# Performance work log

Hardware: AMD Instinct MI355X
Metric: run time of the kernel (lower is better)

The kernel has to match this reference:

```python
import jax, jax.numpy as jnp
import numpy as np

EPS = 1e-5

def _layernorm(x, g, b):
    m = jnp.mean(x, axis=-1, keepdims=True)
    v = jnp.var(x, axis=-1, keepdims=True)
    return (x - m) * jax.lax.rsqrt(v + EPS) * g + b

def setup_inputs() -> dict:
    key = jax.random.key(0)
    ks = jax.random.split(key, 8)
    B, N, D, H = 4, 2048, 1024, 16
    F = 2 * D
    s = 0.02
    return {
        "x": jax.random.normal(ks[0], (B, N, D), jnp.float32),
        "mask": jnp.zeros((B, N, N), jnp.float32),
        "Wq": jax.random.normal(ks[1], (D, D), jnp.float32) * s,
        "Wk": jax.random.normal(ks[2], (D, D), jnp.float32) * s,
        "Wv": jax.random.normal(ks[3], (D, D), jnp.float32) * s,
        "Wc": jax.random.normal(ks[4], (D, D), jnp.float32) * s,
        "bc": jnp.zeros((D,), jnp.float32),
        "W1": jax.random.normal(ks[5], (D, F), jnp.float32) * s,
        "b1": jnp.zeros((F,), jnp.float32),
        "W2": jax.random.normal(ks[6], (F, D), jnp.float32) * s,
        "b2": jnp.zeros((D,), jnp.float32),
        "g1": jnp.ones((D,), jnp.float32),
        "be1": jnp.zeros((D,), jnp.float32),
        "g2": jnp.ones((D,), jnp.float32),
        "be2": jnp.zeros((D,), jnp.float32),
    }

def reference(x, mask, Wq, Wk, Wv, Wc, bc, W1, b1, W2, b2, g1, be1, g2, be2):
    B, N, D = x.shape
    H = 16
    Dh = D // H
    scale = 1.0 / np.sqrt(Dh).astype(np.float32)
    # projections -> [B, H, N, Dh]
    def heads(t):
        return t.reshape(B, N, H, Dh).transpose(0, 2, 1, 3)
    q = heads(x @ Wq)
    k = heads(x @ Wk)
    v = heads(x @ Wv)
    score = jnp.einsum('bhnd,bhmd->bhnm', q, k) * scale + mask[:, None, :, :]
    attn = jnp.einsum('bhnm,bhmd->bhnd', jax.nn.softmax(score, axis=-1), v)
    attn = attn.transpose(0, 2, 1, 3).reshape(B, N, D)
    x = x + attn @ Wc + bc
    x = _layernorm(x, g1, be1)
    x = x + jnp.maximum(x @ W1 + b1, 0.0) @ W2 + b2
    x = _layernorm(x, g2, be2)
    return x
```

## Files before the change

kernel.cpp:

```cpp
#include <hip/hip_runtime.h>
#include <hip/hip_bf16.h>


#define DEV __device__ __forceinline__

using s16x8  = __attribute__((ext_vector_type(8))) short;
using f32x4  = __attribute__((ext_vector_type(4))) float;

DEV unsigned short f2bf(float f) {
  unsigned u = __float_as_uint(f);
  u += 0x7fffu + ((u >> 16) & 1u);
  return (unsigned short)(u >> 16);
}
DEV unsigned cvt_pk_bf16(float lo, float hi) {
  unsigned r;
  asm("v_cvt_pk_bf16_f32 %0, %1, %2" : "=v"(r) : "v"(lo), "v"(hi));
  return r;
}
DEV float bf2f(unsigned short b) { return __uint_as_float((unsigned)b << 16); }

typedef __attribute__((address_space(3))) unsigned lds_u32_t;
typedef const __attribute__((address_space(1))) unsigned glb_u32_t;

DEV void gld_lds16(const void* g, void* l) {
  __builtin_amdgcn_global_load_lds((glb_u32_t*)g, (lds_u32_t*)l, 16, 0, 0);
}

template<int RELU, int VOUT, int SPLITK>
__global__ __launch_bounds__(512, 2)
void gemm8p(const unsigned short* __restrict__ A, const unsigned short* __restrict__ Bt,
            unsigned short* __restrict__ Cb, const float* __restrict__ bias,
            unsigned short* __restrict__ vtout, int M, int N, int K)
{
  __shared__ unsigned short Sh[2][2][256 * 64];
  const int tid = threadIdx.x;
  const int w = tid >> 6, lane = tid & 63;
  const int g = lane >> 4, q = lane & 15;
  const int wr = w >> 2, wc = w & 3;

  const int nwg  = gridDim.x * gridDim.y;
  const int flat = blockIdx.y * gridDim.x + blockIdx.x;
  const int rm   = (flat & 7) * (nwg >> 3) + (flat >> 3);
  int m0, n0, kz = 0;
  if (SPLITK) {
    kz = rm >> 7;
    const int sp = rm & 127;
    m0 = (sp >> 2) * 256; n0 = (sp & 3) * 256;
  } else {
    m0 = (rm / gridDim.x) * 256; n0 = (rm % gridDim.x) * 256;
  }

  f32x4 acc[8][4] = {};

  const int srow = w * 8 + (lane >> 3);
  const int scol = ((lane & 7) ^ (lane >> 3)) * 8;
  const unsigned short* Ag = A  + (size_t)(m0 + srow) * K + scol + (SPLITK ? kz * (K >> 1) : 0);
  const unsigned short* Bg = Bt + (size_t)(n0 + srow) * K + scol + (SPLITK ? kz * (K >> 1) : 0);

  auto STG = [&](const unsigned short* Gb, int buf, int ab, int half, int kt) {
    const unsigned short* gs = Gb + (size_t)(half * 128) * K + kt * 64;
    unsigned short* ls = &Sh[buf][ab][(half * 128 + w * 8) * 64];
    gld_lds16(gs, ls);
    gld_lds16(gs + (size_t)64 * K, ls + 64 * 64);
  };
  auto LDA = [&](int buf, int mq, s16x8 af[4][2]) {
#pragma unroll
    for (int mm = 0; mm < 4; ++mm) {
      const unsigned short* rp = &Sh[buf][0][(wr * 128 + mq * 64 + mm * 16 + q) * 64];
#pragma unroll
      for (int kk = 0; kk < 2; ++kk)
        af[mm][kk] = *(const s16x8*)(rp + (((kk * 4 + g) ^ (q & 7)) * 8));
    }
  };
  auto LDB = [&](int buf, int nq, s16x8 bf[2][2]) {
#pragma unroll
    for (int nn = 0; nn < 2; ++nn) {
      const unsigned short* rp = &Sh[buf][1][(wc * 64 + nq * 32 + nn * 16 + q) * 64];
#pragma unroll
      for (int kk = 0; kk < 2; ++kk)
        bf[nn][kk] = *(const s16x8*)(rp + (((kk * 4 + g) ^ (q & 7)) * 8));
    }
  };
  auto MQ = [&](int mq, int nq, const s16x8 af[4][2], const s16x8 bf[2][2]) {
    __builtin_amdgcn_s_setprio(1);
#pragma unroll
    for (int kk = 0; kk < 2; ++kk)
#pragma unroll
      for (int mm = 0; mm < 4; ++mm)
#pragma unroll
        for (int nn = 0; nn < 2; ++nn)
          acc[mq * 4 + mm][nq * 2 + nn] = __builtin_amdgcn_mfma_f32_16x16x32_bf16(
              af[mm][kk], bf[nn][kk], acc[mq * 4 + mm][nq * 2 + nn], 0, 0, 0);
    __builtin_amdgcn_s_setprio(0);
  };
  auto BAR = [&]() { __builtin_amdgcn_sched_barrier(0); __builtin_amdgcn_s_barrier(); };

  STG(Ag, 0, 0, 0, 0); STG(Ag, 0, 0, 1, 0);
  STG(Bg, 0, 1, 0, 0); STG(Bg, 0, 1, 1, 0);

  const int NKT = SPLITK ? (K >> 7) : (K >> 6);
  s16x8 af[4][2], bf0[2][2], bf1[2][2];
#pragma unroll 1
  for (int kt = 0; kt < NKT; ++kt) {
    const int b = kt & 1, sb = b ^ 1, kn = kt + 1;
    const bool stg = (kn < NKT);
    if (stg) { STG(Ag, sb, 0, 0, kn); asm volatile("s_waitcnt vmcnt(2)" ::: "memory"); }
    else     {                        asm volatile("s_waitcnt vmcnt(0)" ::: "memory"); }
    BAR();
    LDA(b, 0, af); LDB(b, 0, bf0);
    MQ(0, 0, af, bf0);
    BAR();
    if (stg) STG(Ag, sb, 0, 1, kn);
    LDB(b, 1, bf1);
    MQ(0, 1, af, bf1);
    BAR();
    if (stg) STG(Bg, sb, 1, 0, kn);
    LDA(b, 1, af);
    MQ(1, 0, af, bf0);
    BAR();
    if (stg) STG(Bg, sb, 1, 1, kn);
    MQ(1, 1, af, bf1);
    BAR();
  }

#pragma unroll
  for (int n = 0; n < 4; ++n) {
    const int col = n0 + wc * 64 + n * 16 + q;
    if (SPLITK) {
      unsigned short* Cp = Cb + (size_t)kz * M * N;
#pragma unroll
      for (int m = 0; m < 8; ++m) {
        const int row0 = m0 + wr * 128 + m * 16 + g * 4;
#pragma unroll
        for (int r = 0; r < 4; ++r)
          Cp[(size_t)(row0 + r) * N + col] = f2bf(acc[m][n][r]);
      }
    } else if (VOUT && col >= 2048) {
      const int cv = col - 2048;
#pragma unroll
      for (int m = 0; m < 8; ++m) {
        const int row0 = m0 + wr * 128 + m * 16 + g * 4;
        const int bb = row0 >> 11;
        ushort4 pk;
        pk.x = f2bf(acc[m][n][0]); pk.y = f2bf(acc[m][n][1]);
        pk.z = f2bf(acc[m][n][2]); pk.w = f2bf(acc[m][n][3]);
        *(ushort4*)(vtout + ((size_t)bb * 1024 + cv) * 2048 + (row0 & 2047)) = pk;
      }
    } else {
      const float scl = (VOUT && col < 1024) ? 0.18033688011112042f : 1.0f;
      const float bv = bias ? bias[col] : 0.0f;
#pragma unroll
      for (int m = 0; m < 8; ++m) {
        const int row0 = m0 + wr * 128 + m * 16 + g * 4;
#pragma unroll
        for (int r = 0; r < 4; ++r) {
          float v = acc[m][n][r] * scl + bv;
          if (RELU) v = fmaxf(v, 0.0f);
          Cb[(size_t)(row0 + r) * N + col] = f2bf(v);
        }
      }
    }
  }
}

template<int RELU, int RESID, int OUTF>
__global__ __launch_bounds__(256)
void gemm_bt(const unsigned short* __restrict__ A, const unsigned short* __restrict__ Bt,
             unsigned short* __restrict__ Cb, float* __restrict__ Cf,
             const float* __restrict__ bias, const float* __restrict__ resid,
             const unsigned short* __restrict__ residb,
             int M, int N, int K)
{
  __shared__ unsigned short As[2][4096];
  __shared__ unsigned short Bs[2][4096];
  const int tid  = threadIdx.x;
  const int wave = tid >> 6, lane = tid & 63;
  const int g = lane >> 4, q = lane & 15;

  const int nwg  = gridDim.x * gridDim.y;
  const int flat = blockIdx.y * gridDim.x + blockIdx.x;
  const int rm   = (nwg & 7) ? flat : ((flat & 7) * (nwg >> 3) + (flat >> 3));
  const int m0 = (rm / gridDim.x) * 128, n0 = (rm % gridDim.x) * 128;
  const int wr = wave >> 1, wc = wave & 1;

  f32x4 acc[4][4] = {};

  const int i0 = wave * 512 + lane * 8;
  const int i1 = 2048 + i0;

  auto STAGE = [&](int buf, int kt) {
    gld_lds16(A  + (size_t)(m0 + (i0 >> 5)) * K + kt + (i0 & 31), As[buf] + wave * 512);
    gld_lds16(Bt + (size_t)(n0 + (i0 >> 5)) * K + kt + (i0 & 31), Bs[buf] + wave * 512);
    gld_lds16(A  + (size_t)(m0 + (i1 >> 5)) * K + kt + (i1 & 31), As[buf] + 2048 + wave * 512);
    gld_lds16(Bt + (size_t)(n0 + (i1 >> 5)) * K + kt + (i1 & 31), Bs[buf] + 2048 + wave * 512);
  };

  STAGE(0, 0);
  __syncthreads();
  int cur = 0;
#pragma unroll 1
  for (int kt = 0; kt < K; kt += 32) {
    if (kt + 32 < K) STAGE(cur ^ 1, kt + 32);
    s16x8 a[4], b[4];
#pragma unroll
    for (int m = 0; m < 4; ++m)
      a[m] = *(const s16x8*)(As[cur] + (wr * 64 + m * 16 + q) * 32 + g * 8);
#pragma unroll
    for (int n = 0; n < 4; ++n)
      b[n] = *(const s16x8*)(Bs[cur] + (wc * 64 + n * 16 + q) * 32 + g * 8);
    __builtin_amdgcn_s_setprio(1);
#pragma unroll
    for (int m = 0; m < 4; ++m)
#pragma unroll
      for (int n = 0; n < 4; ++n)
        acc[m][n] = __builtin_amdgcn_mfma_f32_16x16x32_bf16(a[m], b[n], acc[m][n], 0, 0, 0);
    __builtin_amdgcn_s_setprio(0);
    __syncthreads();
    cur ^= 1;
  }

#pragma unroll
  for (int n = 0; n < 4; ++n) {
    const int col = n0 + wc * 64 + n * 16 + q;
    const float bv = bias ? bias[col] : 0.0f;
#pragma unroll
    for (int m = 0; m < 4; ++m) {
      const int row0 = m0 + wr * 64 + m * 16 + g * 4;
#pragma unroll
      for (int r = 0; r < 4; ++r) {
        float v = acc[m][n][r] + bv;
        if (RELU) v = fmaxf(v, 0.0f);
        if (RESID == 2) v += bf2f(residb[(size_t)(row0 + r) * N + col]);
        if (OUTF) Cf[(size_t)(row0 + r) * N + col] = v;
        else      Cb[(size_t)(row0 + r) * N + col] = f2bf(v);
      }
    }
  }
}

__global__ __launch_bounds__(256, 4)
void attn_kernel(const unsigned short* __restrict__ qkv,
                 const unsigned short* __restrict__ vt,
                 const float* __restrict__ mask,
                 unsigned short* __restrict__ outb)
{
  __shared__ unsigned short Ks[2][4096];
  __shared__ unsigned short Vs[2][4096];
  const int tid = threadIdx.x, wave = tid >> 6, lane = tid & 63;
  const int g = lane >> 4, q = lane & 15;

  const int flat = blockIdx.y * 32 + blockIdx.x;
  const int rm   = (flat & 7) * 256 + (flat >> 3);
  const int h  = rm & 15;
  const int qt = (rm >> 4) & 31;
  const int b  = rm >> 9;
  const int qrow = qt * 64 + wave * 16;
  const size_t tok0 = (size_t)b * 2048;

  const unsigned short* Qp = qkv + (tok0 + qrow + q) * 3072 + h * 64;
  const s16x8 bq0 = *(const s16x8*)(Qp + g * 8);
  const s16x8 bq1 = *(const s16x8*)(Qp + 32 + g * 8);
  const float* Mp = mask + ((size_t)b * 2048 + qrow + q) * 2048 + g * 4;

  const int lr = lane >> 3;
  const int sc = (lane & 7) ^ lr;
  const unsigned short* Kg = qkv + tok0 * 3072 + 1024 + h * 64
                           + (size_t)(wave * 16 + lr) * 3072 + sc * 8;
  const unsigned short* Vg = vt + (((size_t)b * 16 + h) * 64 + wave * 16 + lr) * 2048 + sc * 8;
  unsigned short* KsW = Ks[0] + wave * 1024;
  unsigned short* VsW = Vs[0] + wave * 1024;

  s16x8 ones;
#pragma unroll
  for (int j = 0; j < 8; ++j) ones[j] = (short)0x3F80;

  f32x4 ot[4] = {};
  f32x4 sacc = {};
  f32x4 mk0[4], mk1[4];
  const float L2E = 1.4426950408889634f;

  gld_lds16(Kg,            KsW);
  gld_lds16(Kg + 8 * 3072, KsW + 512);
  gld_lds16(Vg,            VsW);
  gld_lds16(Vg + 8 * 2048, VsW + 512);
#pragma unroll
  for (int m2 = 0; m2 < 4; ++m2) {
    const f32x4 r = *(const f32x4*)(Mp + m2 * 16);
#pragma unroll
    for (int i = 0; i < 4; ++i) mk0[m2][i] = fmaf(r[i], L2E, -8.0f);
  }
  __syncthreads();

#define ATTN_TILE(BUF, MKC, MKN, STG)                                          \
  {                                                                            \
    f32x4 mu[4];                                                               \
    if (STG) {                                                                 \
      Kg += 64 * 3072; Vg += 64; Mp += 64;                                     \
      gld_lds16(Kg,            KsW + (BUF ^ 1) * 4096);                        \
      gld_lds16(Kg + 8 * 3072, KsW + (BUF ^ 1) * 4096 + 512);                  \
      gld_lds16(Vg,            VsW + (BUF ^ 1) * 4096);                        \
      gld_lds16(Vg + 8 * 2048, VsW + (BUF ^ 1) * 4096 + 512);                  \
      mu[0] = *(const f32x4*)(Mp);      mu[1] = *(const f32x4*)(Mp + 16);      \
      mu[2] = *(const f32x4*)(Mp + 32); mu[3] = *(const f32x4*)(Mp + 48);      \
    }                                                                          \
    __builtin_amdgcn_s_setprio(1);                                             \
    _Pragma("unroll")                                                          \
    for (int m2 = 0; m2 < 4; ++m2) {                                           \
      const unsigned short* kp = Ks[BUF] + (m2 * 16 + q) * 64;                 \
      const s16x8 ak0 = *(const s16x8*)(kp + ((g       ^ (q & 7)) * 8));       \
      const s16x8 ak1 = *(const s16x8*)(kp + (((g + 4) ^ (q & 7)) * 8));       \
      MKC[m2] = __builtin_amdgcn_mfma_f32_16x16x32_bf16(ak0, bq0, MKC[m2], 0, 0, 0); \
      MKC[m2] = __builtin_amdgcn_mfma_f32_16x16x32_bf16(ak1, bq1, MKC[m2], 0, 0, 0); \
    }                                                                          \
    __builtin_amdgcn_s_setprio(0);                                             \
    uint2 pkk[4];                                                              \
    _Pragma("unroll")                                                          \
    for (int m2 = 0; m2 < 4; ++m2) {                                           \
      MKC[m2][0] = exp2f(MKC[m2][0]); MKC[m2][1] = exp2f(MKC[m2][1]);          \
      MKC[m2][2] = exp2f(MKC[m2][2]); MKC[m2][3] = exp2f(MKC[m2][3]);          \
      pkk[m2].x = cvt_pk_bf16(MKC[m2][0], MKC[m2][1]);                         \
      pkk[m2].y = cvt_pk_bf16(MKC[m2][2], MKC[m2][3]);                         \
    }                                                                          \
    __builtin_amdgcn_sched_barrier(0);                                         \
    __builtin_amdgcn_s_barrier();           \
    char* Pw = (char*)(&Ks[BUF][0]) + wave * 2048;                             \
    _Pragma("unroll")                                                          \
    for (int m2 = 0; m2 < 4; ++m2) {                                           \
      const int bir  = m2 * 32 + g * 8;                                        \
      const int addr = q * 128 + (((bir >> 4) ^ (q & 7)) << 4) + (bir & 15);   \
      *(uint2*)(Pw + addr) = pkk[m2];                                          \
    }                                                                          \
    __builtin_amdgcn_s_setprio(1);                                             \
    _Pragma("unroll")                                                          \
    for (int kb = 0; kb < 2; ++kb) {                                           \
      const int blk = (kb * 4 + g) ^ (q & 7);                                  \
      const s16x8 pb = *(const s16x8*)(Pw + q * 128 + blk * 16);               \
      sacc = __builtin_amdgcn_mfma_f32_16x16x32_bf16(ones, pb, sacc, 0, 0, 0); \
      _Pragma("unroll")                                                        \
      for (int mm = 0; mm < 4; ++mm) {                                         \
        const s16x8 av = *(const s16x8*)(Vs[BUF] + (mm * 16 + q) * 64 + blk * 8); \
        ot[mm] = __builtin_amdgcn_mfma_f32_16x16x32_bf16(av, pb, ot[mm], 0, 0, 0); \
      }                                                                        \
    }                                                                          \
    __builtin_amdgcn_s_setprio(0);                                             \
    if (STG) {                                                                 \
      _Pragma("unroll")                                                        \
      for (int m2 = 0; m2 < 4; ++m2) {                                         \
        MKN[m2][0] = fmaf(mu[m2][0], L2E, -8.0f);                              \
        MKN[m2][1] = fmaf(mu[m2][1], L2E, -8.0f);                              \
        MKN[m2][2] = fmaf(mu[m2][2], L2E, -8.0f);                              \
        MKN[m2][3] = fmaf(mu[m2][3], L2E, -8.0f);                              \
      }                                                                        \
    }                                                                          \
    __syncthreads();                                                           \
  }

#pragma unroll 1
  for (int tt = 0; tt < 16; ++tt) {
    ATTN_TILE(0, mk0, mk1, true);
    ATTN_TILE(1, mk1, mk0, (tt < 15));
  }
#undef ATTN_TILE

  char* Pw0 = (char*)(&Ks[0][0]) + wave * 2048;
  const float inv = 1.0f / sacc[0];
#pragma unroll
  for (int mm = 0; mm < 4; ++mm) {
    const int bir  = mm * 32 + g * 8;
    const int addr = q * 128 + (((bir >> 4) ^ (q & 7)) << 4) + (bir & 15);
    uint2 pk;
    pk.x = cvt_pk_bf16(ot[mm][0] * inv, ot[mm][1] * inv);
    pk.y = cvt_pk_bf16(ot[mm][2] * inv, ot[mm][3] * inv);
    *(uint2*)(Pw0 + addr) = pk;
  }
#pragma unroll
  for (int p = 0; p < 2; ++p) {
    const int c  = p * 64 + lane;
    const int qq = c >> 3, cc = c & 7;
    const int blk = cc ^ (qq & 7);
    const s16x8 vv = *(const s16x8*)(Pw0 + qq * 128 + blk * 16);
    *(s16x8*)(outb + (tok0 + qrow + qq) * 1024 + h * 64 + cc * 8) = vv;
  }
}

template<int MODE>
__global__ __launch_bounds__(256)
void ln_kernel(const unsigned short* __restrict__ inb,
               const unsigned short* __restrict__ p0, const unsigned short* __restrict__ p1,
               const float* __restrict__ bias, const unsigned short* __restrict__ residb,
               float* __restrict__ outf, unsigned short* __restrict__ outb,
               const float* __restrict__ gam, const float* __restrict__ bet)
{
  __shared__ float red[8];
  const int row = blockIdx.x, tid = threadIdx.x;
  const size_t base = (size_t)row * 1024 + tid * 4;
  f32x4 v;
  if (MODE == 0) {
    const uint2 u = *(const uint2*)(inb + base);
    v[0] = __uint_as_float(u.x << 16); v[1] = __uint_as_float(u.x & 0xffff0000u);
    v[2] = __uint_as_float(u.y << 16); v[3] = __uint_as_float(u.y & 0xffff0000u);
  } else {
    const uint2 a = *(const uint2*)(p0 + base);
    const uint2 c = *(const uint2*)(p1 + base);
    const f32x4 bs = *(const f32x4*)(bias + tid * 4);
    const uint2 u = *(const uint2*)(residb + base);
    v[0] = __uint_as_float(a.x << 16)         + __uint_as_float(c.x << 16)
         + bs[0] + __uint_as_float(u.x << 16);
    v[1] = __uint_as_float(a.x & 0xffff0000u) + __uint_as_float(c.x & 0xffff0000u)
         + bs[1] + __uint_as_float(u.x & 0xffff0000u);
    v[2] = __uint_as_float(a.y << 16)         + __uint_as_float(c.y << 16)
         + bs[2] + __uint_as_float(u.y << 16);
    v[3] = __uint_as_float(a.y & 0xffff0000u) + __uint_as_float(c.y & 0xffff0000u)
         + bs[3] + __uint_as_float(u.y & 0xffff0000u);
  }
  float s  = v[0] + v[1] + v[2] + v[3];
  float ss = v[0]*v[0] + v[1]*v[1] + v[2]*v[2] + v[3]*v[3];
#pragma unroll
  for (int o = 1; o < 64; o <<= 1) { s += __shfl_xor(s, o); ss += __shfl_xor(ss, o); }
  if ((tid & 63) == 0) { red[tid >> 6] = s; red[4 + (tid >> 6)] = ss; }
  __syncthreads();
  s  = red[0] + red[1] + red[2] + red[3];
  ss = red[4] + red[5] + red[6] + red[7];
  const float mean = s * (1.0f / 1024.0f);
  const float var  = ss * (1.0f / 1024.0f) - mean * mean;
  const float rstd = rsqrtf(var + 1e-5f);
  const f32x4 gm = *(const f32x4*)(gam + tid * 4);
  const f32x4 bt = *(const f32x4*)(bet + tid * 4);
  f32x4 o;
#pragma unroll
  for (int j = 0; j < 4; ++j) o[j] = (v[j] - mean) * rstd * gm[j] + bt[j];
  if (outf) *(f32x4*)(outf + base) = o;
  if (outb) {
    uint2 pk; pk.x = cvt_pk_bf16(o[0], o[1]); pk.y = cvt_pk_bf16(o[2], o[3]);
    *(uint2*)(outb + base) = pk;
  }
}

__global__ __launch_bounds__(256)
void prep_kernel(const float* __restrict__ x, unsigned short* __restrict__ xb,
                 const float* __restrict__ Wq, const float* __restrict__ Wk,
                 const float* __restrict__ Wv, const float* __restrict__ Wc,
                 const float* __restrict__ W1, const float* __restrict__ W2,
                 unsigned short* __restrict__ wqkvt, unsigned short* __restrict__ wct,
                 unsigned short* __restrict__ w1t, unsigned short* __restrict__ w2t)
{
  const int bid = blockIdx.x;
  if (bid < 8192) {
    const size_t i = ((size_t)bid * 256 + threadIdx.x) * 4;
    const f32x4 v = *(const f32x4*)(x + i);
    uint2 pk; pk.x = cvt_pk_bf16(v[0], v[1]); pk.y = cvt_pk_bf16(v[2], v[3]);
    *(uint2*)(xb + i) = pk;
    return;
  }
  __shared__ float t[32][33];
  const int t2 = bid - 8192;
  const float* in; unsigned short* out; int R, C, bx, by;
  if (t2 < 4096) {
    const int widx = t2 >> 10, sub = t2 & 1023;
    in  = (widx == 0) ? Wq : (widx == 1) ? Wk : (widx == 2) ? Wv : Wc;
    out = (widx < 3) ? (wqkvt + (size_t)widx * 1024 * 1024) : wct;
    R = 1024; C = 1024; bx = sub & 31; by = sub >> 5;
  } else if (t2 < 6144) {
    const int sub = t2 - 4096;
    in = W1; out = w1t; R = 1024; C = 2048; bx = sub & 63; by = sub >> 6;
  } else {
    const int sub = t2 - 6144;
    in = W2; out = w2t; R = 2048; C = 1024; bx = sub & 31; by = sub >> 5;
  }
  const int tx = threadIdx.x & 31, ty = threadIdx.x >> 5;
  const int c0 = bx * 32, r0 = by * 32;
#pragma unroll
  for (int k = 0; k < 4; ++k)
    t[ty + k * 8][tx] = in[(size_t)(r0 + ty + k * 8) * C + c0 + tx];
  __syncthreads();
#pragma unroll
  for (int k = 0; k < 4; ++k)
    out[(size_t)(c0 + ty + k * 8) * R + r0 + tx] = f2bf(t[tx][ty + k * 8]);
}

extern "C" void kernel_launch(void* const* d_in, const int* in_sizes, int n_in,
                              void* d_out, int out_size, void* d_ws, size_t ws_size,
                              hipStream_t stream)
{
  (void)in_sizes; (void)n_in; (void)out_size; (void)ws_size;
  const float* x   = (const float*)d_in[0];
  const float* msk = (const float*)d_in[1];
  const float* Wq  = (const float*)d_in[2];
  const float* Wk  = (const float*)d_in[3];
  const float* Wv  = (const float*)d_in[4];
  const float* Wc  = (const float*)d_in[5];
  const float* bc  = (const float*)d_in[6];
  const float* W1  = (const float*)d_in[7];
  const float* b1  = (const float*)d_in[8];
  const float* W2  = (const float*)d_in[9];
  const float* b2  = (const float*)d_in[10];
  const float* g1  = (const float*)d_in[11];
  const float* be1 = (const float*)d_in[12];
  const float* g2  = (const float*)d_in[13];
  const float* be2 = (const float*)d_in[14];
  float* out = (float*)d_out;
  char* ws = (char*)d_ws;
  const size_t MB = 1u << 20;
  unsigned short* xb    = (unsigned short*)(ws + 0 * MB);
  unsigned short* wqkvt = (unsigned short*)(ws + 16 * MB);
  unsigned short* wct   = (unsigned short*)(ws + 22 * MB);
  unsigned short* w1t   = (unsigned short*)(ws + 24 * MB);
  unsigned short* w2t   = (unsigned short*)(ws + 28 * MB);
  unsigned short* qkv   = (unsigned short*)(ws + 32 * MB);
  unsigned short* vt    = (unsigned short*)(ws + 80 * MB);
  unsigned short* attnb = (unsigned short*)(ws + 96 * MB);
  unsigned short* y1b   = (unsigned short*)(ws + 112 * MB);
  unsigned short* h1b   = (unsigned short*)(ws + 128 * MB);
  unsigned short* midb  = (unsigned short*)(ws + 32 * MB);
  unsigned short* pffb  = (unsigned short*)(ws + 64 * MB);

  prep_kernel<<<16384, 256, 0, stream>>>(x, xb, Wq, Wk, Wv, Wc, W1, W2,
                                         wqkvt, wct, w1t, w2t);
  gemm8p<0, 1, 0><<<dim3(12, 32), 512, 0, stream>>>(xb, wqkvt, qkv, nullptr, vt,
                                                    8192, 3072, 1024);
  attn_kernel<<<dim3(32, 64), 256, 0, stream>>>(qkv, vt, msk, attnb);
  gemm_bt<0, 2, 0><<<dim3(8, 64), 256, 0, stream>>>(attnb, wct, y1b, nullptr,
                                                    bc, nullptr, xb, 8192, 1024, 1024);
  ln_kernel<0><<<8192, 256, 0, stream>>>(y1b, nullptr, nullptr, nullptr, nullptr,
                                         nullptr, h1b, g1, be1);
  gemm8p<1, 0, 0><<<dim3(8, 32), 512, 0, stream>>>(h1b, w1t, midb, b1, nullptr,
                                                   8192, 2048, 1024);
  gemm8p<0, 0, 1><<<dim3(8, 32), 512, 0, stream>>>(midb, w2t, pffb, nullptr, nullptr,
                                                   8192, 1024, 2048);
  ln_kernel<1><<<8192, 256, 0, stream>>>(nullptr, pffb, pffb + (size_t)8192 * 1024,
                                         b2, h1b, out, nullptr, g2, be2);
}
```

Measured before the change: 397.7 us.

## Widen attention tiles to 8 waves and route out-projection through split-K gemm8p

The attention kernel now uses 512-thread blocks covering 128 query rows. Each wave loads half as much K/V per tile, and each wave gets its own LDS scratch for P, which removes the extra barrier that came from reusing the K buffer. The output projection drops the 128x128 gemm_bt kernel and uses the gemm8p split-K path, writing two partial bf16 halves. A single unified ln_kernel then sums the halves with bias and residual before the layernorm. LDS use per block grows, and the split-K path costs extra write and read traffic for the partials.

```diff
diff --git a/kernel.cpp b/kernel.cpp
--- a/kernel.cpp
+++ b/kernel.cpp
@@ -163,82 +163,7 @@
   }
 }
 
-template<int RELU, int RESID, int OUTF>
-__global__ __launch_bounds__(256)
-void gemm_bt(const unsigned short* __restrict__ A, const unsigned short* __restrict__ Bt,
-             unsigned short* __restrict__ Cb, float* __restrict__ Cf,
-             const float* __restrict__ bias, const float* __restrict__ resid,
-             const unsigned short* __restrict__ residb,
-             int M, int N, int K)
-{
-  __shared__ unsigned short As[2][4096];
-  __shared__ unsigned short Bs[2][4096];
-  const int tid  = threadIdx.x;
-  const int wave = tid >> 6, lane = tid & 63;
-  const int g = lane >> 4, q = lane & 15;
-
-  const int nwg  = gridDim.x * gridDim.y;
-  const int flat = blockIdx.y * gridDim.x + blockIdx.x;
-  const int rm   = (nwg & 7) ? flat : ((flat & 7) * (nwg >> 3) + (flat >> 3));
-  const int m0 = (rm / gridDim.x) * 128, n0 = (rm % gridDim.x) * 128;
-  const int wr = wave >> 1, wc = wave & 1;
-
-  f32x4 acc[4][4] = {};
-
-  const int i0 = wave * 512 + lane * 8;
-  const int i1 = 2048 + i0;
-
-  auto STAGE = [&](int buf, int kt) {
-    gld_lds16(A  + (size_t)(m0 + (i0 >> 5)) * K + kt + (i0 & 31), As[buf] + wave * 512);
-    gld_lds16(Bt + (size_t)(n0 + (i0 >> 5)) * K + kt + (i0 & 31), Bs[buf] + wave * 512);
-    gld_lds16(A  + (size_t)(m0 + (i1 >> 5)) * K + kt + (i1 & 31), As[buf] + 2048 + wave * 512);
-    gld_lds16(Bt + (size_t)(n0 + (i1 >> 5)) * K + kt + (i1 & 31), Bs[buf] + 2048 + wave * 512);
-  };
-
-  STAGE(0, 0);
-  __syncthreads();
-  int cur = 0;
-#pragma unroll 1
-  for (int kt = 0; kt < K; kt += 32) {
-    if (kt + 32 < K) STAGE(cur ^ 1, kt + 32);
-    s16x8 a[4], b[4];
-#pragma unroll
-    for (int m = 0; m < 4; ++m)
-      a[m] = *(const s16x8*)(As[cur] + (wr * 64 + m * 16 + q) * 32 + g * 8);
-#pragma unroll
-    for (int n = 0; n < 4; ++n)
-      b[n] = *(const s16x8*)(Bs[cur] + (wc * 64 + n * 16 + q) * 32 + g * 8);
-    __builtin_amdgcn_s_setprio(1);
-#pragma unroll
-    for (int m = 0; m < 4; ++m)
-#pragma unroll
-      for (int n = 0; n < 4; ++n)
-        acc[m][n] = __builtin_amdgcn_mfma_f32_16x16x32_bf16(a[m], b[n], acc[m][n], 0, 0, 0);
-    __builtin_amdgcn_s_setprio(0);
-    __syncthreads();
-    cur ^= 1;
-  }
-
-#pragma unroll
-  for (int n = 0; n < 4; ++n) {
-    const int col = n0 + wc * 64 + n * 16 + q;
-    const float bv = bias ? bias[col] : 0.0f;
-#pragma unroll
-    for (int m = 0; m < 4; ++m) {
-      const int row0 = m0 + wr * 64 + m * 16 + g * 4;
-#pragma unroll
-      for (int r = 0; r < 4; ++r) {
-        float v = acc[m][n][r] + bv;
-        if (RELU) v = fmaxf(v, 0.0f);
-        if (RESID == 2) v += bf2f(residb[(size_t)(row0 + r) * N + col]);
-        if (OUTF) Cf[(size_t)(row0 + r) * N + col] = v;
-        else      Cb[(size_t)(row0 + r) * N + col] = f2bf(v);
-      }
-    }
-  }
-}
-
-__global__ __launch_bounds__(256, 4)
+__global__ __launch_bounds__(512, 6)
 void attn_kernel(const unsigned short* __restrict__ qkv,
                  const unsigned short* __restrict__ vt,
                  const float* __restrict__ mask,
@@ -246,15 +171,16 @@
 {
   __shared__ unsigned short Ks[2][4096];
   __shared__ unsigned short Vs[2][4096];
+  __shared__ unsigned short Pl[8][1024];
   const int tid = threadIdx.x, wave = tid >> 6, lane = tid & 63;
   const int g = lane >> 4, q = lane & 15;
 
-  const int flat = blockIdx.y * 32 + blockIdx.x;
-  const int rm   = (flat & 7) * 256 + (flat >> 3);
+  const int flat = blockIdx.y * 16 + blockIdx.x;
+  const int rm   = (flat & 7) * 128 + (flat >> 3);
   const int h  = rm & 15;
-  const int qt = (rm >> 4) & 31;
-  const int b  = rm >> 9;
-  const int qrow = qt * 64 + wave * 16;
+  const int qt = (rm >> 4) & 15;
+  const int b  = rm >> 8;
+  const int qrow = qt * 128 + wave * 16;
   const size_t tok0 = (size_t)b * 2048;
 
   const unsigned short* Qp = qkv + (tok0 + qrow + q) * 3072 + h * 64;
@@ -265,10 +191,10 @@
   const int lr = lane >> 3;
   const int sc = (lane & 7) ^ lr;
   const unsigned short* Kg = qkv + tok0 * 3072 + 1024 + h * 64
-                           + (size_t)(wave * 16 + lr) * 3072 + sc * 8;
-  const unsigned short* Vg = vt + (((size_t)b * 16 + h) * 64 + wave * 16 + lr) * 2048 + sc * 8;
-  unsigned short* KsW = Ks[0] + wave * 1024;
-  unsigned short* VsW = Vs[0] + wave * 1024;
+                           + (size_t)(wave * 8 + lr) * 3072 + sc * 8;
+  const unsigned short* Vg = vt + (((size_t)b * 16 + h) * 64 + wave * 8 + lr) * 2048 + sc * 8;
+  unsigned short* KsW = Ks[0] + wave * 512;
+  unsigned short* VsW = Vs[0] + wave * 512;
 
   s16x8 ones;
 #pragma unroll
@@ -277,12 +203,11 @@
   f32x4 ot[4] = {};
   f32x4 sacc = {};
   f32x4 mk0[4], mk1[4];
+  char* Pw = (char*)&Pl[wave][0];
   const float L2E = 1.4426950408889634f;
 
-  gld_lds16(Kg,            KsW);
-  gld_lds16(Kg + 8 * 3072, KsW + 512);
-  gld_lds16(Vg,            VsW);
-  gld_lds16(Vg + 8 * 2048, VsW + 512);
+  gld_lds16(Kg, KsW);
+  gld_lds16(Vg, VsW);
 #pragma unroll
   for (int m2 = 0; m2 < 4; ++m2) {
     const f32x4 r = *(const f32x4*)(Mp + m2 * 16);
@@ -296,10 +221,8 @@
     f32x4 mu[4];                                                               \
     if (STG) {                                                                 \
       Kg += 64 * 3072; Vg += 64; Mp += 64;                                     \
-      gld_lds16(Kg,            KsW + (BUF ^ 1) * 4096);                        \
-      gld_lds16(Kg + 8 * 3072, KsW + (BUF ^ 1) * 4096 + 512);                  \
-      gld_lds16(Vg,            VsW + (BUF ^ 1) * 4096);                        \
-      gld_lds16(Vg + 8 * 2048, VsW + (BUF ^ 1) * 4096 + 512);                  \
+      gld_lds16(Kg, KsW + (BUF ^ 1) * 4096);                                   \
+      gld_lds16(Vg, VsW + (BUF ^ 1) * 4096);                                   \
       mu[0] = *(const f32x4*)(Mp);      mu[1] = *(const f32x4*)(Mp + 16);      \
       mu[2] = *(const f32x4*)(Mp + 32); mu[3] = *(const f32x4*)(Mp + 48);      \
     }                                                                          \
@@ -313,22 +236,16 @@
       MKC[m2] = __builtin_amdgcn_mfma_f32_16x16x32_bf16(ak1, bq1, MKC[m2], 0, 0, 0); \
     }                                                                          \
     __builtin_amdgcn_s_setprio(0);                                             \
-    uint2 pkk[4];                                                              \
     _Pragma("unroll")                                                          \
     for (int m2 = 0; m2 < 4; ++m2) {                                           \
       MKC[m2][0] = exp2f(MKC[m2][0]); MKC[m2][1] = exp2f(MKC[m2][1]);          \
       MKC[m2][2] = exp2f(MKC[m2][2]); MKC[m2][3] = exp2f(MKC[m2][3]);          \
-      pkk[m2].x = cvt_pk_bf16(MKC[m2][0], MKC[m2][1]);                         \
-      pkk[m2].y = cvt_pk_bf16(MKC[m2][2], MKC[m2][3]);                         \
-    }                                                                          \
-    __builtin_amdgcn_sched_barrier(0);                                         \
-    __builtin_amdgcn_s_barrier();           \
-    char* Pw = (char*)(&Ks[BUF][0]) + wave * 2048;                             \
-    _Pragma("unroll")                                                          \
-    for (int m2 = 0; m2 < 4; ++m2) {                                           \
       const int bir  = m2 * 32 + g * 8;                                        \
       const int addr = q * 128 + (((bir >> 4) ^ (q & 7)) << 4) + (bir & 15);   \
-      *(uint2*)(Pw + addr) = pkk[m2];                                          \
+      uint2 pk;                                                                \
+      pk.x = cvt_pk_bf16(MKC[m2][0], MKC[m2][1]);                              \
+      pk.y = cvt_pk_bf16(MKC[m2][2], MKC[m2][3]);                              \
+      *(uint2*)(Pw + addr) = pk;                        \
     }                                                                          \
     __builtin_amdgcn_s_setprio(1);                                             \
     _Pragma("unroll")                                                          \
@@ -352,7 +269,7 @@
         MKN[m2][3] = fmaf(mu[m2][3], L2E, -8.0f);                              \
       }                                                                        \
     }                                                                          \
-    __syncthreads();                                                           \
+    __syncthreads();                            \
   }
 
 #pragma unroll 1
@@ -362,7 +279,6 @@
   }
 #undef ATTN_TILE
 
-  char* Pw0 = (char*)(&Ks[0][0]) + wave * 2048;
   const float inv = 1.0f / sacc[0];
 #pragma unroll
   for (int mm = 0; mm < 4; ++mm) {
@@ -371,22 +287,20 @@
     uint2 pk;
     pk.x = cvt_pk_bf16(ot[mm][0] * inv, ot[mm][1] * inv);
     pk.y = cvt_pk_bf16(ot[mm][2] * inv, ot[mm][3] * inv);
-    *(uint2*)(Pw0 + addr) = pk;
+    *(uint2*)(Pw + addr) = pk;
   }
 #pragma unroll
   for (int p = 0; p < 2; ++p) {
     const int c  = p * 64 + lane;
     const int qq = c >> 3, cc = c & 7;
     const int blk = cc ^ (qq & 7);
-    const s16x8 vv = *(const s16x8*)(Pw0 + qq * 128 + blk * 16);
+    const s16x8 vv = *(const s16x8*)(Pw + qq * 128 + blk * 16);
     *(s16x8*)(outb + (tok0 + qrow + qq) * 1024 + h * 64 + cc * 8) = vv;
   }
 }
 
-template<int MODE>
 __global__ __launch_bounds__(256)
-void ln_kernel(const unsigned short* __restrict__ inb,
-               const unsigned short* __restrict__ p0, const unsigned short* __restrict__ p1,
+void ln_kernel(const unsigned short* __restrict__ p0, const unsigned short* __restrict__ p1,
                const float* __restrict__ bias, const unsigned short* __restrict__ residb,
                float* __restrict__ outf, unsigned short* __restrict__ outb,
                const float* __restrict__ gam, const float* __restrict__ bet)
@@ -394,25 +308,19 @@
   __shared__ float red[8];
   const int row = blockIdx.x, tid = threadIdx.x;
   const size_t base = (size_t)row * 1024 + tid * 4;
+  const uint2 a = *(const uint2*)(p0 + base);
+  const uint2 c = *(const uint2*)(p1 + base);
+  const f32x4 bs = *(const f32x4*)(bias + tid * 4);
+  const uint2 u = *(const uint2*)(residb + base);
   f32x4 v;
-  if (MODE == 0) {
-    const uint2 u = *(const uint2*)(inb + base);
-    v[0] = __uint_as_float(u.x << 16); v[1] = __uint_as_float(u.x & 0xffff0000u);
-    v[2] = __uint_as_float(u.y << 16); v[3] = __uint_as_float(u.y & 0xffff0000u);
-  } else {
-    const uint2 a = *(const uint2*)(p0 + base);
-    const uint2 c = *(const uint2*)(p1 + base);
-    const f32x4 bs = *(const f32x4*)(bias + tid * 4);
-    const uint2 u = *(const uint2*)(residb + base);
-    v[0] = __uint_as_float(a.x << 16)         + __uint_as_float(c.x << 16)
-         + bs[0] + __uint_as_float(u.x << 16);
-    v[1] = __uint_as_float(a.x & 0xffff0000u) + __uint_as_float(c.x & 0xffff0000u)
-         + bs[1] + __uint_as_float(u.x & 0xffff0000u);
-    v[2] = __uint_as_float(a.y << 16)         + __uint_as_float(c.y << 16)
-         + bs[2] + __uint_as_float(u.y << 16);
-    v[3] = __uint_as_float(a.y & 0xffff0000u) + __uint_as_float(c.y & 0xffff0000u)
-         + bs[3] + __uint_as_float(u.y & 0xffff0000u);
-  }
+  v[0] = __uint_as_float(a.x << 16)         + __uint_as_float(c.x << 16)
+       + bs[0] + __uint_as_float(u.x << 16);
+  v[1] = __uint_as_float(a.x & 0xffff0000u) + __uint_as_float(c.x & 0xffff0000u)
+       + bs[1] + __uint_as_float(u.x & 0xffff0000u);
+  v[2] = __uint_as_float(a.y << 16)         + __uint_as_float(c.y << 16)
+       + bs[2] + __uint_as_float(u.y << 16);
+  v[3] = __uint_as_float(a.y & 0xffff0000u) + __uint_as_float(c.y & 0xffff0000u)
+       + bs[3] + __uint_as_float(u.y & 0xffff0000u);
   float s  = v[0] + v[1] + v[2] + v[3];
   float ss = v[0]*v[0] + v[1]*v[1] + v[2]*v[2] + v[3]*v[3];
 #pragma unroll
@@ -509,8 +417,8 @@
   unsigned short* qkv   = (unsigned short*)(ws + 32 * MB);
   unsigned short* vt    = (unsigned short*)(ws + 80 * MB);
   unsigned short* attnb = (unsigned short*)(ws + 96 * MB);
-  unsigned short* y1b   = (unsigned short*)(ws + 112 * MB);
   unsigned short* h1b   = (unsigned short*)(ws + 128 * MB);
+  unsigned short* prb   = (unsigned short*)(ws + 32 * MB);
   unsigned short* midb  = (unsigned short*)(ws + 32 * MB);
   unsigned short* pffb  = (unsigned short*)(ws + 64 * MB);
 
@@ -518,15 +426,15 @@
                                          wqkvt, wct, w1t, w2t);
   gemm8p<0, 1, 0><<<dim3(12, 32), 512, 0, stream>>>(xb, wqkvt, qkv, nullptr, vt,
                                                     8192, 3072, 1024);
-  attn_kernel<<<dim3(32, 64), 256, 0, stream>>>(qkv, vt, msk, attnb);
-  gemm_bt<0, 2, 0><<<dim3(8, 64), 256, 0, stream>>>(attnb, wct, y1b, nullptr,
-                                                    bc, nullptr, xb, 8192, 1024, 1024);
-  ln_kernel<0><<<8192, 256, 0, stream>>>(y1b, nullptr, nullptr, nullptr, nullptr,
-                                         nullptr, h1b, g1, be1);
+  attn_kernel<<<dim3(16, 64), 512, 0, stream>>>(qkv, vt, msk, attnb);
+  gemm8p<0, 0, 1><<<dim3(8, 32), 512, 0, stream>>>(attnb, wct, prb, nullptr, nullptr,
+                                                   8192, 1024, 1024);
+  ln_kernel<<<8192, 256, 0, stream>>>(prb, prb + (size_t)8192 * 1024,
+                                      bc, xb, nullptr, h1b, g1, be1);
   gemm8p<1, 0, 0><<<dim3(8, 32), 512, 0, stream>>>(h1b, w1t, midb, b1, nullptr,
                                                    8192, 2048, 1024);
   gemm8p<0, 0, 1><<<dim3(8, 32), 512, 0, stream>>>(midb, w2t, pffb, nullptr, nullptr,
                                                    8192, 1024, 2048);
-  ln_kernel<1><<<8192, 256, 0, stream>>>(nullptr, pffb, pffb + (size_t)8192 * 1024,
-                                         b2, h1b, out, nullptr, g2, be2);
-}
+  ln_kernel<<<8192, 256, 0, stream>>>(pffb, pffb + (size_t)8192 * 1024,
+                                      b2, h1b, out, nullptr, g2, be2);
+}
```

After: 838.5 us. 2.11x slower.
